# Optimization experiments

Hardware: AMD Instinct MI355X
Metric: run time of the kernel (lower is better)

Reference implementation:

```python
import jax, jax.numpy as jnp
import numpy as np


def setup_inputs() -> dict:
    key = jax.random.key(0)
    k1, k2, k3, k4 = jax.random.split(key, 4)
    B, I, P, F = 4096, 1024, 512, 2048
    x = jax.random.normal(k1, (B, I), dtype=jnp.float32)
    # params initialized like torch.rand(...)*2-1 (uniform in [-1,1])
    features = jax.random.uniform(k2, (F, I), dtype=jnp.float32, minval=-1.0, maxval=1.0)
    prototypes = jax.random.uniform(k3, (P, I), dtype=jnp.float32, minval=-1.0, maxval=1.0)
    # scalars: torch inits to zeros; use small nonzero values so output/grads are informative
    abt = jax.random.normal(k4, (3,), dtype=jnp.float32) * 0.1
    alpha = abt[0:1]
    beta = abt[1:2]
    theta = abt[2:3]
    return {"x": x, "features": features, "prototypes": prototypes,
            "alpha": alpha, "beta": beta, "theta": theta}


def reference(x, features, prototypes, alpha, beta, theta):
    # x: [b, i], features: [f, i], prototypes: [p, i]
    # Original einsums broadcast over p but the projection is p-independent:
    xf = x @ features.T            # [b, f]
    pf = prototypes @ features.T   # [p, f]
    x_pres = jax.nn.relu(xf)       # [b, f]
    p_pres = jax.nn.relu(pf)       # [p, f]
    # common[b,p]       = sum_f xf*pf*relu(xf)*relu(pf)
    # x_distinct[b,p]   = sum_f xf*relu(xf)*(1-relu(pf))
    # p_distinct[b,p]   = sum_f pf*relu(pf)*(1-relu(xf))
    a = xf * x_pres                # [b, f]
    c = pf * p_pres                # [p, f]
    common = a @ c.T                                   # [b, p]
    x_distinctive = a @ (1.0 - p_pres).T               # [b, p]
    p_distinctive = (1.0 - x_pres) @ c.T               # [b, p]
    return theta * common - alpha * x_distinctive - beta * p_distinctive
```

## Files before the change

### kernel.cpp

```cpp
#include <hip/hip_runtime.h>
#include <cstdint>

typedef __attribute__((ext_vector_type(8))) short bf16x8;
typedef __attribute__((ext_vector_type(16))) float f32x16;
typedef __attribute__((ext_vector_type(4))) float f4;
typedef __attribute__((ext_vector_type(8))) unsigned short u16x8;
typedef unsigned short u16;


__device__ __forceinline__ u16 f2bf(float f) {
  uint32_t u = __builtin_bit_cast(uint32_t, f);
  u += 0x7fffu + ((u >> 16) & 1u);
  return (u16)(u >> 16);
}

__device__ __forceinline__ float bf2f(u16 h) {
  return __builtin_bit_cast(float, (uint32_t)h << 16);
}

__device__ __forceinline__ void async_cp16(const void* g, void* l) {
  __builtin_amdgcn_global_load_lds(
      (const __attribute__((address_space(1))) uint32_t*)g,
      (__attribute__((address_space(3))) uint32_t*)l, 16, 0, 0);
}

__global__ __launch_bounds__(256) void cast3(
    const float* __restrict__ x, const float* __restrict__ f,
    const float* __restrict__ p, u16* __restrict__ dst,
    int n1, int n2, int n3) {
  int i = (blockIdx.x * 256 + threadIdx.x) * 8;
  const float* src;
  int local;
  if (i < n1) { src = x; local = i; }
  else if (i < n1 + n2) { src = f; local = i - n1; }
  else if (i < n1 + n2 + n3) { src = p; local = i - n1 - n2; }
  else return;
  f4 a = *(const f4*)(src + local);
  f4 b = *(const f4*)(src + local + 4);
  u16x8 o;
  o[0] = f2bf(a.x); o[1] = f2bf(a.y); o[2] = f2bf(a.z); o[3] = f2bf(a.w);
  o[4] = f2bf(b.x); o[5] = f2bf(b.y); o[6] = f2bf(b.z); o[7] = f2bf(b.w);
  *(u16x8*)(dst + i) = o;
}

__device__ __forceinline__ void mainloop(
    const u16* __restrict__ A, const u16* __restrict__ B, int K,
    int kbeg, int kend, int tid, u16* lds, f32x16 (&acc)[2][2]) {
  constexpr int TM = 128, TN = 128, BK = 64;
  const int lane = tid & 63;
  const int wave = tid >> 6;
  const int wrow = wave >> 1, wcol = wave & 1;

  for (int k0 = kbeg; k0 < kend; k0 += BK) {
    #pragma unroll
    for (int it = 0; it < TM / 32; ++it) {
      int c = it * 256 + tid;
      int row = c >> 3, pc = c & 7;
      int gc = pc ^ (row & 7);
      async_cp16(A + (size_t)row * K + (k0 + gc * 8),
                 &lds[(it * 256 + wave * 64) * 8]);
    }
    #pragma unroll
    for (int it = 0; it < TN / 32; ++it) {
      int c = it * 256 + tid;
      int row = c >> 3, pc = c & 7;
      int gc = pc ^ (row & 7);
      async_cp16(B + (size_t)row * K + (k0 + gc * 8),
                 &lds[TM * 64 + (it * 256 + wave * 64) * 8]);
    }
    __syncthreads();

    #pragma unroll
    for (int s = 0; s < 4; ++s) {
      const int h = s * 2 + (lane >> 5);
      bf16x8 bfr[2], afr[2];
      #pragma unroll
      for (int j = 0; j < 2; ++j) {
        const int rb = wcol * 64 + j * 32 + (lane & 31);
        bfr[j] = *(const bf16x8*)&lds[TM * 64 + (rb * 8 + (h ^ (rb & 7))) * 8];
      }
      #pragma unroll
      for (int i = 0; i < 2; ++i) {
        const int ra = wrow * 64 + i * 32 + (lane & 31);
        afr[i] = *(const bf16x8*)&lds[(ra * 8 + (h ^ (ra & 7))) * 8];
      }
      #pragma unroll
      for (int i = 0; i < 2; ++i)
        #pragma unroll
        for (int j = 0; j < 2; ++j)
          acc[i][j] = __builtin_amdgcn_mfma_f32_32x32x16_bf16(
              afr[i], bfr[j], acc[i][j], 0, 0, 0);
    }
    __syncthreads();
  }
}


__global__ __launch_bounds__(256) void gemm12(
    const u16* __restrict__ xb, const u16* __restrict__ pb,
    const u16* __restrict__ fb, u16* __restrict__ Acat, u16* __restrict__ Bcat,
    const float* __restrict__ alpha, const float* __restrict__ beta,
    const float* __restrict__ theta) {
  constexpr int TM = 128, TN = 128, K = 1024, N = 2048;
  constexpr int TSTRIDE = 136;
  __shared__ u16 lds[17408];

  const int tid = threadIdx.x;
  const int lane = tid & 63;
  const int wave = tid >> 6;
  const int wrow = wave >> 1, wcol = wave & 1;
  const int bm_all = blockIdx.x * TM;
  const int bn = blockIdx.y * TN;
  const bool is_x = bm_all < 4096;
  const u16* A = is_x ? xb + (size_t)bm_all * K : pb + (size_t)(bm_all - 4096) * K;
  const u16* B = fb + (size_t)bn * K;

  f32x16 acc[2][2] = {};
  mainloop(A, B, K, 0, K, tid, lds, acc);

  float th = 0.f, al = 0.f, be = 0.f;
  if (!is_x) { th = theta[0]; al = alpha[0]; be = beta[0]; }
  u16* dst = is_x ? Acat : Bcat;
  const int rowbase = is_x ? bm_all : bm_all - 4096;
  const int rquad = 4 * (lane >> 5);

  #pragma unroll
  for (int half = 0; half < 2; ++half) {
    __syncthreads();
    #pragma unroll
    for (int i = 0; i < 2; ++i) {
      #pragma unroll
      for (int j = 0; j < 2; ++j) {
        const int cl = wcol * 64 + j * 32 + (lane & 31);
        #pragma unroll
        for (int r = 0; r < 16; ++r) {
          const int rl = wrow * 64 + i * 32 + (r & 3) + 8 * (r >> 2) + rquad;
          float v = acc[i][j][r];
          float pres = v > 0.f ? v : 0.f;
          float o;
          if (is_x) o = half == 0 ? v * pres : 1.f - pres;
          else {
            float cc = v * pres;
            o = half == 0 ? th * cc - al * (1.f - pres) : -be * cc;
          }
          lds[rl * TSTRIDE + cl] = f2bf(o);
        }
      }
    }
    __syncthreads();
    #pragma unroll
    for (int v = 0; v < 8; ++v) {
      const int rl = v * 16 + (tid >> 4);
      const int c8 = (tid & 15) * 8;
      u16x8 vec = *(const u16x8*)&lds[rl * TSTRIDE + c8];
      *(u16x8*)&dst[(size_t)(rowbase + rl) * (2 * N) + bn + c8 + half * N] = vec;
    }
  }
}

__global__ __launch_bounds__(256) void gemm3(
    const u16* __restrict__ Acat, const u16* __restrict__ Bcat,
    u16* __restrict__ part) {
  constexpr int TM = 128, TN = 128, K = 4096, KSPLIT = 4;
  __shared__ u16 lds[16384];

  const int tid = threadIdx.x;
  const int bm = blockIdx.x * TM;
  const int bn = blockIdx.y * TN;
  const int kbeg = blockIdx.z * (K / KSPLIT);
  const int kend = kbeg + (K / KSPLIT);

  f32x16 acc[2][2] = {};
  mainloop(Acat + (size_t)bm * K, Bcat + (size_t)bn * K, K, kbeg, kend,
           tid, lds, acc);

  const size_t pbase =
      ((size_t)blockIdx.z * 128 + blockIdx.y * 32 + blockIdx.x) * 16384;
  #pragma unroll
  for (int i = 0; i < 2; ++i)
    #pragma unroll
    for (int j = 0; j < 2; ++j)
      #pragma unroll
      for (int h = 0; h < 2; ++h) {
        u16x8 o;
        #pragma unroll
        for (int e = 0; e < 8; ++e) o[e] = f2bf(acc[i][j][h * 8 + e]);
        *(u16x8*)&part[pbase + (size_t)(i * 4 + j * 2 + h) * 2048 + tid * 8] = o;
      }
}

__global__ __launch_bounds__(256) void reduce4(
    const u16* __restrict__ part, float* __restrict__ out) {
  constexpr int N = 512;
  const int tid = threadIdx.x;
  const int lane = tid & 63;
  const int wave = tid >> 6;
  const int wrow = wave >> 1, wcol = wave & 1;
  const int tileId = blockIdx.x >> 3;
  const int q = blockIdx.x & 7;
  const int bm = (tileId & 31) * 128;
  const int bn = (tileId >> 5) * 128;

  float v[8] = {};
  #pragma unroll
  for (int z = 0; z < 4; ++z) {
    u16x8 u = *(const u16x8*)&part[((size_t)z * 128 + tileId) * 16384 +
                                   (size_t)q * 2048 + tid * 8];
    #pragma unroll
    for (int e = 0; e < 8; ++e) v[e] += bf2f(u[e]);
  }
  const int i = q >> 2, j = (q >> 1) & 1, h = q & 1;
  const int gc = bn + wcol * 64 + j * 32 + (lane & 31);
  const int grb = bm + wrow * 64 + i * 32 + 4 * (lane >> 5);
  #pragma unroll
  for (int e = 0; e < 8; ++e) {
    const int reg = h * 8 + e;
    out[(size_t)(grb + (reg & 3) + 8 * (reg >> 2)) * N + gc] = v[e];
  }
}

extern "C" void kernel_launch(void* const* d_in, const int* in_sizes, int n_in,
                              void* d_out, int out_size, void* d_ws, size_t ws_size,
                              hipStream_t stream) {
  const float* x     = (const float*)d_in[0];
  const float* feat  = (const float*)d_in[1];
  const float* proto = (const float*)d_in[2];
  const float* alpha = (const float*)d_in[3];
  const float* beta  = (const float*)d_in[4];
  const float* theta = (const float*)d_in[5];
  float* out = (float*)d_out;

  constexpr int Bb = 4096, Ii = 1024, Pp = 512, Ff = 2048;

  char* ws = (char*)d_ws;
  u16* xb   = (u16*)ws;
  u16* fb   = xb + (size_t)Bb * Ii;
  u16* pb   = fb + (size_t)Ff * Ii;
  size_t r0 = 33554432;
  u16* Acat = (u16*)(ws + r0);
  u16* Bcat = Acat + (size_t)Bb * 2 * Ff;
  u16* part = Bcat + (size_t)Pp * 2 * Ff;

  const int n1 = Bb * Ii, n2 = Ff * Ii, n3 = Pp * Ii;
  cast3<<<((n1 + n2 + n3) / 8 + 255) / 256, 256, 0, stream>>>(
      x, feat, proto, xb, n1, n2, n3);

  gemm12<<<dim3(36, 16), 256, 0, stream>>>(xb, pb, fb, Acat, Bcat, alpha, beta, theta);

  gemm3<<<dim3(Bb / 128, Pp / 128, 4), 256, 0, stream>>>(Acat, Bcat, part);

  reduce4<<<1024, 256, 0, stream>>>(part, out);
}
```

Baseline: 147.0 us.

## Double-buffer LDS tiles to overlap global loads with MFMA compute

The GEMM mainloop now stages the next K tile into a second LDS buffer with async global-to-LDS copies while the current tile is computed. It uses a partial vmcnt wait and raw barriers instead of a full sync before each tile. The goal is to hide global memory latency behind matrix work. LDS per block doubles to 64KB, which may reduce occupancy, and correctness relies on the hand-set vmcnt count matching the 8 outstanding loads.

```diff
diff --git a/kernel.cpp b/kernel.cpp
--- a/kernel.cpp
+++ b/kernel.cpp
@@ -43,55 +43,78 @@
   *(u16x8*)(dst + i) = o;
 }
 
+
+__device__ __forceinline__ void stage_tile(
+    const u16* __restrict__ A, const u16* __restrict__ B, int K,
+    int k0, int tid, u16* L) {
+  constexpr int TM = 128, TN = 128;
+  const int wave = tid >> 6;
+  #pragma unroll
+  for (int it = 0; it < TM / 32; ++it) {
+    int c = it * 256 + tid;
+    int row = c >> 3, pc = c & 7;
+    int gc = pc ^ (row & 7);
+    async_cp16(A + (size_t)row * K + (k0 + gc * 8),
+               &L[(it * 256 + wave * 64) * 8]);
+  }
+  #pragma unroll
+  for (int it = 0; it < TN / 32; ++it) {
+    int c = it * 256 + tid;
+    int row = c >> 3, pc = c & 7;
+    int gc = pc ^ (row & 7);
+    async_cp16(B + (size_t)row * K + (k0 + gc * 8),
+               &L[TM * 64 + (it * 256 + wave * 64) * 8]);
+  }
+}
+
+__device__ __forceinline__ void compute_tile(
+    const u16* L, int lane, int wrow, int wcol, f32x16 (&acc)[2][2]) {
+  constexpr int TM = 128;
+  #pragma unroll
+  for (int s = 0; s < 4; ++s) {
+    const int h = s * 2 + (lane >> 5);
+    bf16x8 bfr[2], afr[2];
+    #pragma unroll
+    for (int j = 0; j < 2; ++j) {
+      const int rb = wcol * 64 + j * 32 + (lane & 31);
+      bfr[j] = *(const bf16x8*)&L[TM * 64 + (rb * 8 + (h ^ (rb & 7))) * 8];
+    }
+    #pragma unroll
+    for (int i = 0; i < 2; ++i) {
+      const int ra = wrow * 64 + i * 32 + (lane & 31);
+      afr[i] = *(const bf16x8*)&L[(ra * 8 + (h ^ (ra & 7))) * 8];
+    }
+    #pragma unroll
+    for (int i = 0; i < 2; ++i)
+      #pragma unroll
+      for (int j = 0; j < 2; ++j)
+        acc[i][j] = __builtin_amdgcn_mfma_f32_32x32x16_bf16(
+            afr[i], bfr[j], acc[i][j], 0, 0, 0);
+  }
+}
+
 __device__ __forceinline__ void mainloop(
     const u16* __restrict__ A, const u16* __restrict__ B, int K,
     int kbeg, int kend, int tid, u16* lds, f32x16 (&acc)[2][2]) {
-  constexpr int TM = 128, TN = 128, BK = 64;
+  constexpr int BK = 64;
+  constexpr int BUF = 16384;
   const int lane = tid & 63;
   const int wave = tid >> 6;
   const int wrow = wave >> 1, wcol = wave & 1;
 
+  stage_tile(A, B, K, kbeg, tid, lds);
+  int cur = 0;
   for (int k0 = kbeg; k0 < kend; k0 += BK) {
-    #pragma unroll
-    for (int it = 0; it < TM / 32; ++it) {
-      int c = it * 256 + tid;
-      int row = c >> 3, pc = c & 7;
-      int gc = pc ^ (row & 7);
-      async_cp16(A + (size_t)row * K + (k0 + gc * 8),
-                 &lds[(it * 256 + wave * 64) * 8]);
-    }
-    #pragma unroll
-    for (int it = 0; it < TN / 32; ++it) {
-      int c = it * 256 + tid;
-      int row = c >> 3, pc = c & 7;
-      int gc = pc ^ (row & 7);
-      async_cp16(B + (size_t)row * K + (k0 + gc * 8),
-                 &lds[TM * 64 + (it * 256 + wave * 64) * 8]);
-    }
-    __syncthreads();
-
-    #pragma unroll
-    for (int s = 0; s < 4; ++s) {
-      const int h = s * 2 + (lane >> 5);
-      bf16x8 bfr[2], afr[2];
-      #pragma unroll
-      for (int j = 0; j < 2; ++j) {
-        const int rb = wcol * 64 + j * 32 + (lane & 31);
-        bfr[j] = *(const bf16x8*)&lds[TM * 64 + (rb * 8 + (h ^ (rb & 7))) * 8];
-      }
-      #pragma unroll
-      for (int i = 0; i < 2; ++i) {
-        const int ra = wrow * 64 + i * 32 + (lane & 31);
-        afr[i] = *(const bf16x8*)&lds[(ra * 8 + (h ^ (ra & 7))) * 8];
-      }
-      #pragma unroll
-      for (int i = 0; i < 2; ++i)
-        #pragma unroll
-        for (int j = 0; j < 2; ++j)
-          acc[i][j] = __builtin_amdgcn_mfma_f32_32x32x16_bf16(
-              afr[i], bfr[j], acc[i][j], 0, 0, 0);
-    }
-    __syncthreads();
+    if (k0 + BK < kend) {
+      stage_tile(A, B, K, k0 + BK, tid, lds + (cur ^ 1) * BUF);
+      asm volatile("s_waitcnt vmcnt(8)" ::: "memory");
+    } else {
+      asm volatile("s_waitcnt vmcnt(0)" ::: "memory");
+    }
+    __builtin_amdgcn_s_barrier();
+    compute_tile(lds + cur * BUF, lane, wrow, wcol, acc);
+    __builtin_amdgcn_s_barrier();
+    cur ^= 1;
   }
 }
 
@@ -101,16 +124,16 @@
     const u16* __restrict__ fb, u16* __restrict__ Acat, u16* __restrict__ Bcat,
     const float* __restrict__ alpha, const float* __restrict__ beta,
     const float* __restrict__ theta) {
-  constexpr int TM = 128, TN = 128, K = 1024, N = 2048;
+  constexpr int TM = 128, K = 1024, N = 2048;
   constexpr int TSTRIDE = 136;
-  __shared__ u16 lds[17408];
+  __shared__ u16 lds[32768];
 
   const int tid = threadIdx.x;
   const int lane = tid & 63;
   const int wave = tid >> 6;
   const int wrow = wave >> 1, wcol = wave & 1;
   const int bm_all = blockIdx.x * TM;
-  const int bn = blockIdx.y * TN;
+  const int bn = blockIdx.y * 128;
   const bool is_x = bm_all < 4096;
   const u16* A = is_x ? xb + (size_t)bm_all * K : pb + (size_t)(bm_all - 4096) * K;
   const u16* B = fb + (size_t)bn * K;
@@ -162,7 +185,7 @@
     const u16* __restrict__ Acat, const u16* __restrict__ Bcat,
     u16* __restrict__ part) {
   constexpr int TM = 128, TN = 128, K = 4096, KSPLIT = 4;
-  __shared__ u16 lds[16384];
+  __shared__ u16 lds[32768];
 
   const int tid = threadIdx.x;
   const int bm = blockIdx.x * TM;
```

Result: faster. 139.7 us (-4.9%).
